# Optimization experiments

Measured on AMD Instinct MI355X. Metric: run time of the kernel, lower is better.

Reference implementation:

```python
import jax, jax.numpy as jnp
import numpy as np

S, E, H, D, F = 2048, 1280, 16, 80, 5120
EPS = 1e-6


def _ln(x, g, b):
    m = x.mean(-1, keepdims=True)
    v = x.var(-1, keepdims=True)
    return (x - m) * jax.lax.rsqrt(v + EPS) * g + b


def _rotate_half(x):
    x1, x2 = jnp.split(x, 2, axis=-1)
    return jnp.concatenate([-x2, x1], axis=-1)


def _quick_gelu(x):
    return x * jax.nn.sigmoid(1.702 * x)


def setup_inputs() -> dict:
    key = jax.random.key(0)
    ks = jax.random.split(key, 12)
    inp = {
        "hidden_states": jax.random.normal(ks[0], (S, E), jnp.float32),
        "attention_mask": jnp.ones((1, 1, S, S), jnp.bool_),
        "cos": jax.random.uniform(ks[1], (S, D), jnp.float32),
        "sin": jax.random.uniform(ks[2], (S, D), jnp.float32),
        "ln1_g": jnp.ones((E,), jnp.float32),
        "ln1_b": jnp.zeros((E,), jnp.float32),
        "ln2_g": jnp.ones((E,), jnp.float32),
        "ln2_b": jnp.zeros((E,), jnp.float32),
        "w_qkv": jax.random.normal(ks[3], (E, 3 * E), jnp.float32) * (E ** -0.5),
        "b_qkv": jax.random.normal(ks[4], (3 * E,), jnp.float32) * 0.02,
        "w_o": jax.random.normal(ks[5], (E, E), jnp.float32) * (E ** -0.5),
        "b_o": jax.random.normal(ks[6], (E,), jnp.float32) * 0.02,
        "w_fc1": jax.random.normal(ks[7], (E, F), jnp.float32) * (E ** -0.5),
        "b_fc1": jax.random.normal(ks[8], (F,), jnp.float32) * 0.02,
        "w_fc2": jax.random.normal(ks[9], (F, E), jnp.float32) * (F ** -0.5),
        "b_fc2": jax.random.normal(ks[10], (E,), jnp.float32) * 0.02,
    }
    return inp


def reference(hidden_states, attention_mask, cos, sin, ln1_g, ln1_b, ln2_g, ln2_b,
              w_qkv, b_qkv, w_o, b_o, w_fc1, b_fc1, w_fc2, b_fc2):
    x = hidden_states  # [S, E]
    h = _ln(x, ln1_g, ln1_b)
    qkv = h @ w_qkv + b_qkv  # [S, 3E]
    q, k, v = jnp.split(qkv, 3, axis=-1)
    q = q.reshape(S, H, D)
    k = k.reshape(S, H, D)
    v = v.reshape(S, H, D)
    # rotary in fp32, cos/sin broadcast over head axis: [S, 1, D]
    c = cos[:, None, :].astype(jnp.float32)
    s = sin[:, None, :].astype(jnp.float32)
    qf, kf = q.astype(jnp.float32), k.astype(jnp.float32)
    q = (qf * c + _rotate_half(qf) * s).astype(q.dtype)
    k = (kf * c + _rotate_half(kf) * s).astype(k.dtype)
    # attention scores [H, S, S]
    scores = jnp.einsum('shd,thd->hst', q, k) / np.float32(np.sqrt(D))
    scores = jnp.where(attention_mask[0], scores, jnp.finfo(scores.dtype).min)
    probs = jax.nn.softmax(scores.astype(jnp.float32), axis=-1).astype(q.dtype)
    attn = jnp.einsum('hst,thd->shd', probs, v).reshape(S, E)
    attn = attn @ w_o + b_o
    x = x + attn
    h2 = _ln(x, ln2_g, ln2_b)
    mlp = _quick_gelu(h2 @ w_fc1 + b_fc1) @ w_fc2 + b_fc2
    return x + mlp
```

## Files before the change

kernel.cpp:

```cpp
#include <hip/hip_runtime.h>
#include <stdint.h>
#include <math.h>

#define S_LEN 2048
#define EMB   1280
#define NHEAD 16
#define HDIM  80
#define FDIM  5120

typedef __bf16 bf16x8 __attribute__((ext_vector_type(8)));
typedef float  f32x4  __attribute__((ext_vector_type(4)));
typedef int    i32x4  __attribute__((ext_vector_type(4)));
typedef unsigned short u16x8 __attribute__((ext_vector_type(8)));
typedef unsigned short u16x4 __attribute__((ext_vector_type(4)));

__device__ __forceinline__ float b2f(unsigned short u) {
    union { float f; unsigned int i; } x; x.i = ((unsigned int)u) << 16; return x.f;
}
__device__ __forceinline__ unsigned short f2b(float f) {
    union { float f; unsigned int i; } x; x.f = f;
    unsigned int r = x.i + 0x7FFFu + ((x.i >> 16) & 1u);
    return (unsigned short)(r >> 16);
}

__device__ __forceinline__ float wave_rsum(float v) {
    #pragma unroll
    for (int o = 32; o; o >>= 1) v += __shfl_down(v, o);
    return v;
}

typedef const __attribute__((address_space(1))) unsigned int* as1_u32p;
typedef __attribute__((address_space(3))) unsigned int* as3_u32p;
__device__ __forceinline__ void gload16(const unsigned short* g, unsigned short* l) {
    __builtin_amdgcn_global_load_lds((as1_u32p)g, (as3_u32p)l, 16, 0, 0);
}

__global__ __launch_bounds__(256) void transpose_conv_kernel(
    const float* __restrict__ in, unsigned short* __restrict__ out,
    int R, int C)
{
    __shared__ unsigned short tile[64][65];
    int c0 = blockIdx.x * 64, r0 = blockIdx.y * 64;
    int tx = threadIdx.x & 63, ty = threadIdx.x >> 6;
    #pragma unroll
    for (int j = 0; j < 16; ++j) {
        int row = ty + j * 4;
        tile[row][tx] = f2b(in[(size_t)(r0 + row) * C + c0 + tx]);
    }
    __syncthreads();
    #pragma unroll
    for (int j = 0; j < 16; ++j) {
        int row = ty + j * 4;
        out[(size_t)(c0 + row) * R + r0 + tx] = tile[tx][row];
    }
}

__global__ __launch_bounds__(256) void ln_kernel(
    const float* __restrict__ x,
    const float* __restrict__ g,
    const float* __restrict__ b,
    unsigned short* __restrict__ out)
{
    int row = blockIdx.x, tid = threadIdx.x;
    int lane = tid & 63, wave = tid >> 6;
    const float* xr = x + (size_t)row * EMB;
    float v[5], s = 0.f, ss = 0.f;
    #pragma unroll
    for (int i = 0; i < 5; ++i) {
        float f = xr[tid + i * 256];
        v[i] = f; s += f; ss += f * f;
    }
    s = wave_rsum(s); ss = wave_rsum(ss);
    __shared__ float rs[4], rss[4];
    if (lane == 0) { rs[wave] = s; rss[wave] = ss; }
    __syncthreads();
    float st  = rs[0] + rs[1] + rs[2] + rs[3];
    float sst = rss[0] + rss[1] + rss[2] + rss[3];
    float mean = st * (1.0f / EMB);
    float var  = sst * (1.0f / EMB) - mean * mean;
    float inv  = rsqrtf(var + 1e-6f);
    unsigned short* orow = out + (size_t)row * EMB;
    #pragma unroll
    for (int i = 0; i < 5; ++i) {
        int c = tid + i * 256;
        orow[c] = f2b((v[i] - mean) * inv * g[c] + b[c]);
    }
}

template<int EPI, int OM, int NT, int SPLIT>
__global__ __launch_bounds__(256) void gemm_kernel(
    const unsigned short* __restrict__ A,
    const unsigned short* __restrict__ Bt,
    const float* __restrict__ bias,
    const float* __restrict__ res,
    void* __restrict__ Cv,
    int M, int N, int K)
{
    __shared__ __align__(16) unsigned short As[2][128 * 32];
    __shared__ __align__(16) unsigned short Bs[2][NT * 32 * 32];

    int tid = threadIdx.x;
    int lane = tid & 63, wave = tid >> 6;
    int m0 = blockIdx.x * 128, n0 = blockIdx.y * (NT * 32);
    int wm = (wave >> 1) * 64, wn = (wave & 1) * (NT * 16);
    int kc = K / SPLIT;
    int kbeg = blockIdx.z * kc;

    f32x4 acc[4][NT];
    #pragma unroll
    for (int i = 0; i < 4; ++i)
        #pragma unroll
        for (int j = 0; j < NT; ++j)
            acc[i][j] = (f32x4){0.f, 0.f, 0.f, 0.f};

    const unsigned short* Ap0 = A  + (size_t)(m0 + (tid >> 2)) * K + (tid & 3) * 8 + kbeg;
    const unsigned short* Ap1 = Ap0 + (size_t)64 * K;
    const unsigned short* Bp0 = Bt + (size_t)(n0 + (tid >> 2)) * K + (tid & 3) * 8 + kbeg;
    const unsigned short* Bp1 = Bp0 + (size_t)64 * K;

    int arow = lane & 15, aq = (lane >> 4) * 8;
    int aoff[4], boff[NT];
    #pragma unroll
    for (int i = 0; i < 4; ++i)
        aoff[i] = (wm + i * 16 + arow) * 32 + aq;
    #pragma unroll
    for (int i = 0; i < NT; ++i)
        boff[i] = (wn + i * 16 + arow) * 32 + aq;

    for (int k0 = 0; k0 < kc; k0 += 64) {
        __syncthreads();
        gload16(Ap0 + k0,      &As[0][tid * 8]);
        gload16(Ap1 + k0,      &As[0][2048 + tid * 8]);
        gload16(Bp0 + k0,      &Bs[0][tid * 8]);
        if (NT == 4) gload16(Bp1 + k0, &Bs[0][2048 + tid * 8]);
        gload16(Ap0 + k0 + 32, &As[1][tid * 8]);
        gload16(Ap1 + k0 + 32, &As[1][2048 + tid * 8]);
        gload16(Bp0 + k0 + 32, &Bs[1][tid * 8]);
        if (NT == 4) gload16(Bp1 + k0 + 32, &Bs[1][2048 + tid * 8]);
        __syncthreads();

        #pragma unroll
        for (int p = 0; p < 2; ++p) {
            bf16x8 af[4], bfm[NT];
            #pragma unroll
            for (int i = 0; i < 4; ++i)
                af[i] = *(const bf16x8*)&As[p][aoff[i]];
            #pragma unroll
            for (int i = 0; i < NT; ++i)
                bfm[i] = *(const bf16x8*)&Bs[p][boff[i]];
            #pragma unroll
            for (int mi = 0; mi < 4; ++mi)
                #pragma unroll
                for (int ni = 0; ni < NT; ++ni)
                    acc[mi][ni] = __builtin_amdgcn_mfma_f32_16x16x32_bf16(
                        af[mi], bfm[ni], acc[mi][ni], 0, 0, 0);
        }
    }

    int col = lane & 15;
    int rbase = (lane >> 4) * 4;
    #pragma unroll
    for (int ni = 0; ni < NT; ++ni) {
        int gn = n0 + wn + ni * 16 + col;
        float bv = (OM == 2) ? 0.f : bias[gn];
        #pragma unroll
        for (int mi = 0; mi < 4; ++mi) {
            int gm = m0 + wm + mi * 16 + rbase;
            #pragma unroll
            for (int r = 0; r < 4; ++r) {
                float v = acc[mi][ni][r] + bv;
                if (OM != 2) {
                    if (EPI == 1) v = v / (1.0f + expf(-1.702f * v));
                    if (EPI == 2) v += res[(size_t)(gm + r) * N + gn];
                }
                if (OM == 2)
                    ((float*)Cv)[((size_t)blockIdx.z * M + gm + r) * N + gn] = v;
                else if (OM == 1)
                    ((float*)Cv)[(size_t)(gm + r) * N + gn] = v;
                else
                    ((unsigned short*)Cv)[(size_t)(gm + r) * N + gn] = f2b(v);
            }
        }
    }
}

__global__ __launch_bounds__(256) void reduce4_kernel(
    const float* __restrict__ part,
    const float* __restrict__ res,
    const float* __restrict__ bias,
    float* __restrict__ out)
{
    size_t i4 = ((size_t)blockIdx.x * 256 + threadIdx.x) * 4;
    int colb = (int)(i4 % EMB);
    f32x4 a = *(const f32x4*)&res[i4];
    f32x4 bv = *(const f32x4*)&bias[colb];
    a += bv;
    const size_t slice = (size_t)S_LEN * EMB;
    #pragma unroll
    for (int z = 0; z < 4; ++z)
        a += *(const f32x4*)&part[z * slice + i4];
    *(f32x4*)&out[i4] = a;
}

__global__ __launch_bounds__(256) void ropev_kernel(
    const unsigned short* __restrict__ qkv,
    const float* __restrict__ cosb,
    const float* __restrict__ sinb,
    unsigned short* __restrict__ q_out,
    unsigned short* __restrict__ k_out,
    unsigned short* __restrict__ vt)
{
    __shared__ unsigned short qT[64 * 84];
    __shared__ unsigned short kT[64 * 84];
    __shared__ unsigned short vT[64 * 84];

    int h = blockIdx.x >> 5, stile = blockIdx.x & 31;
    int s0 = stile * 64;
    int tid = threadIdx.x;

    u16x4 qr[5], kr[5];
    #pragma unroll
    for (int i = 0; i < 5; ++i) {
        int u = tid + i * 256;
        int row = u / 20, col = (u % 20) * 4;
        const unsigned short* base = qkv + (size_t)(s0 + row) * (3 * EMB) + h * HDIM + col;
        qr[i] = *(const u16x4*)base;
        kr[i] = *(const u16x4*)(base + EMB);
        u16x4 v4 = *(const u16x4*)(base + 2 * EMB);
        *(u16x4*)&qT[row * 84 + col] = qr[i];
        *(u16x4*)&kT[row * 84 + col] = kr[i];
        *(u16x4*)&vT[row * 84 + col] = v4;
    }
    __syncthreads();

    #pragma unroll
    for (int i = 0; i < 5; ++i) {
        int u = tid + i * 256;
        int row = u / 20, col = (u % 20) * 4;
        int pcol = (col < 40) ? col + 40 : col - 40;
        float sgn = (col < 40) ? -1.f : 1.f;
        u16x4 qp = *(const u16x4*)&qT[row * 84 + pcol];
        u16x4 kp = *(const u16x4*)&kT[row * 84 + pcol];
        f32x4 c4 = *(const f32x4*)&cosb[(size_t)(s0 + row) * HDIM + col];
        f32x4 s4 = *(const f32x4*)&sinb[(size_t)(s0 + row) * HDIM + col];
        u16x4 qo, ko;
        #pragma unroll
        for (int j = 0; j < 4; ++j) {
            qo[j] = f2b(b2f(qr[i][j]) * c4[j] + sgn * b2f(qp[j]) * s4[j]);
            ko[j] = f2b(b2f(kr[i][j]) * c4[j] + sgn * b2f(kp[j]) * s4[j]);
        }
        size_t o = ((size_t)h * S_LEN + s0 + row) * HDIM + col;
        *(u16x4*)&q_out[o] = qo;
        *(u16x4*)&k_out[o] = ko;
    }
    #pragma unroll
    for (int i = 0; i < 5; ++i) {
        int w = tid + i * 256;
        int d = w >> 4, c4i = (w & 15) * 4;
        u16x4 pk;
        #pragma unroll
        for (int j = 0; j < 4; ++j) pk[j] = vT[(c4i + j) * 84 + d];
        *(u16x4*)(vt + ((size_t)h * HDIM + d) * S_LEN + s0 + c4i) = pk;
    }
}

__global__ __launch_bounds__(256) void fattn_kernel(
    const unsigned short* __restrict__ q,
    const unsigned short* __restrict__ k,
    const unsigned short* __restrict__ vt,
    unsigned short* __restrict__ out)
{
    __shared__ __align__(16) unsigned short Qs[64 * 96];
    __shared__ __align__(16) unsigned short Ks[2][64 * 96];
    __shared__ __align__(16) unsigned short Vs[2][80 * 72];
    __shared__ __align__(16) unsigned short Pt[4 * 16 * 72];

    int tid = threadIdx.x;
    int lane = tid & 63, wave = tid >> 6;
    int arow = lane & 15, quad = lane >> 4;
    int h = blockIdx.x >> 5, qb = blockIdx.x & 31;
    int s0 = qb * 64;
    const float c = 0.16129856f;

    const unsigned short* qbase = q + ((size_t)h * S_LEN + s0) * HDIM;
    const unsigned short* kbase = k + (size_t)h * S_LEN * HDIM;
    const unsigned short* vbase = vt + (size_t)h * HDIM * S_LEN;

    #pragma unroll
    for (int i = 0; i < 5; ++i) {
        int u = tid + i * 256;
        int row = u / 20, col = (u % 20) * 4;
        *(u16x4*)&Qs[row * 96 + col] = *(const u16x4*)(qbase + u * 4);
    }
    {
        int zr = tid >> 2, zc = 80 + (tid & 3) * 4;
        *(u16x4*)&Qs[zr * 96 + zc]    = (u16x4){0, 0, 0, 0};
        *(u16x4*)&Ks[0][zr * 96 + zc] = (u16x4){0, 0, 0, 0};
        *(u16x4*)&Ks[1][zr * 96 + zc] = (u16x4){0, 0, 0, 0};
    }

    u16x4 kreg[5], vreg[5];
    #pragma unroll
    for (int i = 0; i < 5; ++i) {
        int u = tid + i * 256;
        kreg[i] = *(const u16x4*)(kbase + u * 4);
        vreg[i] = *(const u16x4*)(vbase + (size_t)(u >> 4) * S_LEN + (u & 15) * 4);
    }
    #pragma unroll
    for (int i = 0; i < 5; ++i) {
        int u = tid + i * 256;
        *(u16x4*)&Ks[0][(u / 20) * 96 + (u % 20) * 4] = kreg[i];
        *(u16x4*)&Vs[0][(u >> 4) * 72 + (u & 15) * 4] = vreg[i];
    }
    #pragma unroll
    for (int i = 0; i < 5; ++i) {
        int u = tid + i * 256;
        kreg[i] = *(const u16x4*)(kbase + (size_t)64 * HDIM + u * 4);
        vreg[i] = *(const u16x4*)(vbase + (size_t)(u >> 4) * S_LEN + 64 + (u & 15) * 4);
    }
    __syncthreads();

    int pw = wave * 16 * 72;
    float m_run = -3e38f;
    float l_run = 0.f;
    f32x4 o[5];
    #pragma unroll
    for (int di = 0; di < 5; ++di) o[di] = (f32x4){0.f, 0.f, 0.f, 0.f};

    const int NIT = S_LEN / 64;
    for (int it = 0; it < NIT; ++it) {
        int cur = it & 1;
        if (it + 1 < NIT) {
            int nb = (it + 1) & 1;
            #pragma unroll
            for (int i = 0; i < 5; ++i) {
                int u = tid + i * 256;
                *(u16x4*)&Ks[nb][(u / 20) * 96 + (u % 20) * 4] = kreg[i];
                *(u16x4*)&Vs[nb][(u >> 4) * 72 + (u & 15) * 4] = vreg[i];
            }
        }
        if (it + 2 < NIT) {
            int t0 = (it + 2) * 64;
            #pragma unroll
            for (int i = 0; i < 5; ++i) {
                int u = tid + i * 256;
                kreg[i] = *(const u16x4*)(kbase + (size_t)t0 * HDIM + u * 4);
                vreg[i] = *(const u16x4*)(vbase + (size_t)(u >> 4) * S_LEN + t0 + (u & 15) * 4);
            }
        }

        f32x4 sc[4];
        #pragma unroll
        for (int ni = 0; ni < 4; ++ni) sc[ni] = (f32x4){0.f, 0.f, 0.f, 0.f};
        #pragma unroll
        for (int kk = 0; kk < 3; ++kk) {
            bf16x8 bq = *(const bf16x8*)&Qs[(wave * 16 + arow) * 96 + kk * 32 + quad * 8];
            #pragma unroll
            for (int ni = 0; ni < 4; ++ni) {
                bf16x8 ak = *(const bf16x8*)&Ks[cur][(ni * 16 + arow) * 96 + kk * 32 + quad * 8];
                sc[ni] = __builtin_amdgcn_mfma_f32_16x16x32_bf16(ak, bq, sc[ni], 0, 0, 0);
            }
        }

        float tm = -3e38f;
        #pragma unroll
        for (int ni = 0; ni < 4; ++ni)
            #pragma unroll
            for (int r = 0; r < 4; ++r) tm = fmaxf(tm, sc[ni][r]);
        tm = fmaxf(tm, __shfl_xor(tm, 16));
        tm = fmaxf(tm, __shfl_xor(tm, 32));
        float mn = fmaxf(m_run, tm);
        float alpha = exp2f((m_run - mn) * c);
        m_run = mn;
        float mc = mn * c;
        float rs = 0.f;
        #pragma unroll
        for (int ni = 0; ni < 4; ++ni) {
            #pragma unroll
            for (int r = 0; r < 4; ++r) {
                float p = exp2f(sc[ni][r] * c - mc);
                sc[ni][r] = p;
                rs += p;
            }
        }
        rs += __shfl_xor(rs, 16);
        rs += __shfl_xor(rs, 32);
        l_run = l_run * alpha + rs;

        #pragma unroll
        for (int ni = 0; ni < 4; ++ni) {
            u16x4 pk;
            #pragma unroll
            for (int r = 0; r < 4; ++r) {
                __bf16 pb = (__bf16)sc[ni][r];
                pk[r] = *(unsigned short*)&pb;
            }
            *(u16x4*)&Pt[pw + arow * 72 + ni * 16 + quad * 4] = pk;
        }

        float al[4];
        #pragma unroll
        for (int r = 0; r < 4; ++r)
            al[r] = __shfl(alpha, (lane & 48) | (quad * 4 + r));
        #pragma unroll
        for (int di = 0; di < 5; ++di)
            #pragma unroll
            for (int r = 0; r < 4; ++r) o[di][r] *= al[r];

        #pragma unroll
        for (int kk = 0; kk < 2; ++kk) {
            bf16x8 ap = *(const bf16x8*)&Pt[pw + arow * 72 + kk * 32 + quad * 8];
            #pragma unroll
            for (int di = 0; di < 5; ++di) {
                bf16x8 bv = *(const bf16x8*)&Vs[cur][(di * 16 + arow) * 72 + kk * 32 + quad * 8];
                o[di] = __builtin_amdgcn_mfma_f32_16x16x32_bf16(ap, bv, o[di], 0, 0, 0);
            }
        }

        __syncthreads();
    }

    float inv[4];
    #pragma unroll
    for (int r = 0; r < 4; ++r)
        inv[r] = 1.f / __shfl(l_run, (lane & 48) | (quad * 4 + r));
    #pragma unroll
    for (int r = 0; r < 4; ++r) {
        int gq = s0 + wave * 16 + quad * 4 + r;
        unsigned short* op = out + (size_t)gq * EMB + h * HDIM;
        #pragma unroll
        for (int di = 0; di < 5; ++di)
            op[di * 16 + arow] = f2b(o[di][r] * inv[r]);
    }
}

extern "C" void kernel_launch(void* const* d_in, const int* in_sizes, int n_in,
                              void* d_out, int out_size, void* d_ws, size_t ws_size,
                              hipStream_t stream)
{
    const float* hidden = (const float*)d_in[0];
    const float* cosb  = (const float*)d_in[2];
    const float* sinb  = (const float*)d_in[3];
    const float* ln1g  = (const float*)d_in[4];
    const float* ln1b  = (const float*)d_in[5];
    const float* ln2g  = (const float*)d_in[6];
    const float* ln2b  = (const float*)d_in[7];
    const float* w_qkv = (const float*)d_in[8];
    const float* b_qkv = (const float*)d_in[9];
    const float* w_o   = (const float*)d_in[10];
    const float* b_o   = (const float*)d_in[11];
    const float* w_fc1 = (const float*)d_in[12];
    const float* b_fc1 = (const float*)d_in[13];
    const float* w_fc2 = (const float*)d_in[14];
    const float* b_fc2 = (const float*)d_in[15];

    char* ws = (char*)d_ws;
    size_t off = 0;
    auto alloc = [&](size_t bytes) -> void* {
        void* p = (void*)(ws + off);
        off += (bytes + 255) & ~(size_t)255;
        return p;
    };
    unsigned short* wT_qkv = (unsigned short*)alloc((size_t)3840 * 1280 * 2);
    unsigned short* wT_o   = (unsigned short*)alloc((size_t)1280 * 1280 * 2);
    unsigned short* wT_fc1 = (unsigned short*)alloc((size_t)5120 * 1280 * 2);
    unsigned short* wT_fc2 = (unsigned short*)alloc((size_t)1280 * 5120 * 2);
    unsigned short* h1     = (unsigned short*)alloc((size_t)S_LEN * EMB * 2);
    unsigned short* qkv    = (unsigned short*)alloc((size_t)S_LEN * 3 * EMB * 2);
    unsigned short* q_r    = (unsigned short*)alloc((size_t)S_LEN * EMB * 2);
    unsigned short* k_r    = (unsigned short*)alloc((size_t)S_LEN * EMB * 2);
    unsigned short* vt_g   = (unsigned short*)alloc((size_t)S_LEN * EMB * 2);
    unsigned short* attn_o = (unsigned short*)alloc((size_t)S_LEN * EMB * 2);
    float*          x1     = (float*)alloc((size_t)S_LEN * EMB * 4);
    unsigned short* h2     = (unsigned short*)alloc((size_t)S_LEN * EMB * 2);
    unsigned short* mlp1   = (unsigned short*)alloc((size_t)S_LEN * FDIM * 2);
    float* fc2part = (float*)h1;

    transpose_conv_kernel<<<dim3(3840 / 64, 1280 / 64), 256, 0, stream>>>(w_qkv, wT_qkv, 1280, 3840);
    transpose_conv_kernel<<<dim3(1280 / 64, 1280 / 64), 256, 0, stream>>>(w_o,   wT_o,   1280, 1280);
    transpose_conv_kernel<<<dim3(5120 / 64, 1280 / 64), 256, 0, stream>>>(w_fc1, wT_fc1, 1280, 5120);
    transpose_conv_kernel<<<dim3(1280 / 64, 5120 / 64), 256, 0, stream>>>(w_fc2, wT_fc2, 5120, 1280);

    ln_kernel<<<S_LEN, 256, 0, stream>>>(hidden, ln1g, ln1b, h1);

    gemm_kernel<0, 0, 4, 1><<<dim3(S_LEN / 128, 3840 / 128, 1), 256, 0, stream>>>(
        h1, wT_qkv, b_qkv, nullptr, qkv, S_LEN, 3 * EMB, EMB);

    ropev_kernel<<<NHEAD * (S_LEN / 64), 256, 0, stream>>>(qkv, cosb, sinb, q_r, k_r, vt_g);

    fattn_kernel<<<NHEAD * (S_LEN / 64), 256, 0, stream>>>(q_r, k_r, vt_g, attn_o);

    gemm_kernel<2, 1, 2, 1><<<dim3(S_LEN / 128, 1280 / 64, 1), 256, 0, stream>>>(
        attn_o, wT_o, b_o, hidden, x1, S_LEN, EMB, EMB);

    ln_kernel<<<S_LEN, 256, 0, stream>>>(x1, ln2g, ln2b, h2);

    gemm_kernel<1, 0, 4, 1><<<dim3(S_LEN / 128, FDIM / 128, 1), 256, 0, stream>>>(
        h2, wT_fc1, b_fc1, nullptr, mlp1, S_LEN, FDIM, EMB);

    gemm_kernel<0, 2, 4, 4><<<dim3(S_LEN / 128, 1280 / 128, 4), 256, 0, stream>>>(
        mlp1, wT_fc2, b_fc2, nullptr, fc2part, S_LEN, EMB, FDIM);
    reduce4_kernel<<<(S_LEN * EMB / 4) / 256, 256, 0, stream>>>(
        fc2part, x1, b_fc2, (float*)d_out);
}
```

Baseline: 406.3 us.

## Merge weight transposes, shrink GEMM N-tile to 64, split-K the output projection

The four weight-transpose launches become one kernel that dispatches blocks by index range, removing launch overhead. The GEMM template drops the NT parameter and always uses a 128x64 tile, which doubles grid sizes for the QKV, FC1 and FC2 GEMMs to raise occupancy across CUs, at the cost of less A-tile reuse per block. The output projection now uses split-K=2 writing fp32 partials, followed by a reduce kernel that adds bias and the residual. That adds a partial-buffer round trip and one extra launch.

```diff
diff --git a/kernel.cpp b/kernel.cpp
--- a/kernel.cpp
+++ b/kernel.cpp
@@ -35,13 +35,13 @@
     __builtin_amdgcn_global_load_lds((as1_u32p)g, (as3_u32p)l, 16, 0, 0);
 }
 
-__global__ __launch_bounds__(256) void transpose_conv_kernel(
+__device__ __forceinline__ void trans64(
     const float* __restrict__ in, unsigned short* __restrict__ out,
-    int R, int C)
+    int R, int C, int bx, int by, int tid)
 {
     __shared__ unsigned short tile[64][65];
-    int c0 = blockIdx.x * 64, r0 = blockIdx.y * 64;
-    int tx = threadIdx.x & 63, ty = threadIdx.x >> 6;
+    int c0 = bx * 64, r0 = by * 64;
+    int tx = tid & 63, ty = tid >> 6;
     #pragma unroll
     for (int j = 0; j < 16; ++j) {
         int row = ty + j * 4;
@@ -52,6 +52,27 @@
     for (int j = 0; j < 16; ++j) {
         int row = ty + j * 4;
         out[(size_t)(c0 + row) * R + r0 + tx] = tile[tx][row];
+    }
+}
+
+__global__ __launch_bounds__(256) void transpose4_kernel(
+    const float* __restrict__ w_qkv, unsigned short* __restrict__ wT_qkv,
+    const float* __restrict__ w_o,   unsigned short* __restrict__ wT_o,
+    const float* __restrict__ w_fc1, unsigned short* __restrict__ wT_fc1,
+    const float* __restrict__ w_fc2, unsigned short* __restrict__ wT_fc2)
+{
+    int id = blockIdx.x, tid = threadIdx.x;
+    if (id < 1200) {
+        trans64(w_qkv, wT_qkv, 1280, 3840, id % 60, id / 60, tid);
+    } else if (id < 1600) {
+        int t = id - 1200;
+        trans64(w_o, wT_o, 1280, 1280, t % 20, t / 20, tid);
+    } else if (id < 3200) {
+        int t = id - 1600;
+        trans64(w_fc1, wT_fc1, 1280, 5120, t % 80, t / 80, tid);
+    } else {
+        int t = id - 3200;
+        trans64(w_fc2, wT_fc2, 5120, 1280, t % 20, t / 20, tid);
     }
 }
 
@@ -87,7 +108,7 @@
     }
 }
 
-template<int EPI, int OM, int NT, int SPLIT>
+template<int EPI, int OM, int SPLIT>
 __global__ __launch_bounds__(256) void gemm_kernel(
     const unsigned short* __restrict__ A,
     const unsigned short* __restrict__ Bt,
@@ -97,34 +118,33 @@
     int M, int N, int K)
 {
     __shared__ __align__(16) unsigned short As[2][128 * 32];
-    __shared__ __align__(16) unsigned short Bs[2][NT * 32 * 32];
+    __shared__ __align__(16) unsigned short Bs[2][64 * 32];
 
     int tid = threadIdx.x;
     int lane = tid & 63, wave = tid >> 6;
-    int m0 = blockIdx.x * 128, n0 = blockIdx.y * (NT * 32);
-    int wm = (wave >> 1) * 64, wn = (wave & 1) * (NT * 16);
+    int m0 = blockIdx.x * 128, n0 = blockIdx.y * 64;
+    int wm = (wave >> 1) * 64, wn = (wave & 1) * 32;
     int kc = K / SPLIT;
     int kbeg = blockIdx.z * kc;
 
-    f32x4 acc[4][NT];
+    f32x4 acc[4][2];
     #pragma unroll
     for (int i = 0; i < 4; ++i)
         #pragma unroll
-        for (int j = 0; j < NT; ++j)
+        for (int j = 0; j < 2; ++j)
             acc[i][j] = (f32x4){0.f, 0.f, 0.f, 0.f};
 
     const unsigned short* Ap0 = A  + (size_t)(m0 + (tid >> 2)) * K + (tid & 3) * 8 + kbeg;
     const unsigned short* Ap1 = Ap0 + (size_t)64 * K;
     const unsigned short* Bp0 = Bt + (size_t)(n0 + (tid >> 2)) * K + (tid & 3) * 8 + kbeg;
-    const unsigned short* Bp1 = Bp0 + (size_t)64 * K;
 
     int arow = lane & 15, aq = (lane >> 4) * 8;
-    int aoff[4], boff[NT];
+    int aoff[4], boff[2];
     #pragma unroll
     for (int i = 0; i < 4; ++i)
         aoff[i] = (wm + i * 16 + arow) * 32 + aq;
     #pragma unroll
-    for (int i = 0; i < NT; ++i)
+    for (int i = 0; i < 2; ++i)
         boff[i] = (wn + i * 16 + arow) * 32 + aq;
 
     for (int k0 = 0; k0 < kc; k0 += 64) {
@@ -132,26 +152,24 @@
         gload16(Ap0 + k0,      &As[0][tid * 8]);
         gload16(Ap1 + k0,      &As[0][2048 + tid * 8]);
         gload16(Bp0 + k0,      &Bs[0][tid * 8]);
-        if (NT == 4) gload16(Bp1 + k0, &Bs[0][2048 + tid * 8]);
         gload16(Ap0 + k0 + 32, &As[1][tid * 8]);
         gload16(Ap1 + k0 + 32, &As[1][2048 + tid * 8]);
         gload16(Bp0 + k0 + 32, &Bs[1][tid * 8]);
-        if (NT == 4) gload16(Bp1 + k0 + 32, &Bs[1][2048 + tid * 8]);
         __syncthreads();
 
         #pragma unroll
         for (int p = 0; p < 2; ++p) {
-            bf16x8 af[4], bfm[NT];
+            bf16x8 af[4], bfm[2];
             #pragma unroll
             for (int i = 0; i < 4; ++i)
                 af[i] = *(const bf16x8*)&As[p][aoff[i]];
             #pragma unroll
-            for (int i = 0; i < NT; ++i)
+            for (int i = 0; i < 2; ++i)
                 bfm[i] = *(const bf16x8*)&Bs[p][boff[i]];
             #pragma unroll
             for (int mi = 0; mi < 4; ++mi)
                 #pragma unroll
-                for (int ni = 0; ni < NT; ++ni)
+                for (int ni = 0; ni < 2; ++ni)
                     acc[mi][ni] = __builtin_amdgcn_mfma_f32_16x16x32_bf16(
                         af[mi], bfm[ni], acc[mi][ni], 0, 0, 0);
         }
@@ -160,7 +178,7 @@
     int col = lane & 15;
     int rbase = (lane >> 4) * 4;
     #pragma unroll
-    for (int ni = 0; ni < NT; ++ni) {
+    for (int ni = 0; ni < 2; ++ni) {
         int gn = n0 + wn + ni * 16 + col;
         float bv = (OM == 2) ? 0.f : bias[gn];
         #pragma unroll
@@ -184,7 +202,8 @@
     }
 }
 
-__global__ __launch_bounds__(256) void reduce4_kernel(
+template<int Z>
+__global__ __launch_bounds__(256) void reduceZ_kernel(
     const float* __restrict__ part,
     const float* __restrict__ res,
     const float* __restrict__ bias,
@@ -197,7 +216,7 @@
     a += bv;
     const size_t slice = (size_t)S_LEN * EMB;
     #pragma unroll
-    for (int z = 0; z < 4; ++z)
+    for (int z = 0; z < Z; ++z)
         a += *(const f32x4*)&part[z * slice + i4];
     *(f32x4*)&out[i4] = a;
 }
@@ -474,32 +493,32 @@
     float*          x1     = (float*)alloc((size_t)S_LEN * EMB * 4);
     unsigned short* h2     = (unsigned short*)alloc((size_t)S_LEN * EMB * 2);
     unsigned short* mlp1   = (unsigned short*)alloc((size_t)S_LEN * FDIM * 2);
-    float* fc2part = (float*)h1;
-
-    transpose_conv_kernel<<<dim3(3840 / 64, 1280 / 64), 256, 0, stream>>>(w_qkv, wT_qkv, 1280, 3840);
-    transpose_conv_kernel<<<dim3(1280 / 64, 1280 / 64), 256, 0, stream>>>(w_o,   wT_o,   1280, 1280);
-    transpose_conv_kernel<<<dim3(5120 / 64, 1280 / 64), 256, 0, stream>>>(w_fc1, wT_fc1, 1280, 5120);
-    transpose_conv_kernel<<<dim3(1280 / 64, 5120 / 64), 256, 0, stream>>>(w_fc2, wT_fc2, 5120, 1280);
+    float* partials = (float*)h1;
+
+    transpose4_kernel<<<4800, 256, 0, stream>>>(
+        w_qkv, wT_qkv, w_o, wT_o, w_fc1, wT_fc1, w_fc2, wT_fc2);
 
     ln_kernel<<<S_LEN, 256, 0, stream>>>(hidden, ln1g, ln1b, h1);
 
-    gemm_kernel<0, 0, 4, 1><<<dim3(S_LEN / 128, 3840 / 128, 1), 256, 0, stream>>>(
+    gemm_kernel<0, 0, 1><<<dim3(S_LEN / 128, 3840 / 64, 1), 256, 0, stream>>>(
         h1, wT_qkv, b_qkv, nullptr, qkv, S_LEN, 3 * EMB, EMB);
 
     ropev_kernel<<<NHEAD * (S_LEN / 64), 256, 0, stream>>>(qkv, cosb, sinb, q_r, k_r, vt_g);
 
     fattn_kernel<<<NHEAD * (S_LEN / 64), 256, 0, stream>>>(q_r, k_r, vt_g, attn_o);
 
-    gemm_kernel<2, 1, 2, 1><<<dim3(S_LEN / 128, 1280 / 64, 1), 256, 0, stream>>>(
-        attn_o, wT_o, b_o, hidden, x1, S_LEN, EMB, EMB);
+    gemm_kernel<0, 2, 2><<<dim3(S_LEN / 128, 1280 / 64, 2), 256, 0, stream>>>(
+        attn_o, wT_o, b_o, nullptr, partials, S_LEN, EMB, EMB);
+    reduceZ_kernel<2><<<(S_LEN * EMB / 4) / 256, 256, 0, stream>>>(
+        partials, hidden, b_o, x1);
 
     ln_kernel<<<S_LEN, 256, 0, stream>>>(x1, ln2g, ln2b, h2);
 
-    gemm_kernel<1, 0, 4, 1><<<dim3(S_LEN / 128, FDIM / 128, 1), 256, 0, stream>>>(
+    gemm_kernel<1, 0, 1><<<dim3(S_LEN / 128, FDIM / 64, 1), 256, 0, stream>>>(
         h2, wT_fc1, b_fc1, nullptr, mlp1, S_LEN, FDIM, EMB);
 
-    gemm_kernel<0, 2, 4, 4><<<dim3(S_LEN / 128, 1280 / 128, 4), 256, 0, stream>>>(
-        mlp1, wT_fc2, b_fc2, nullptr, fc2part, S_LEN, EMB, FDIM);
-    reduce4_kernel<<<(S_LEN * EMB / 4) / 256, 256, 0, stream>>>(
-        fc2part, x1, b_fc2, (float*)d_out);
-}
+    gemm_kernel<0, 2, 4><<<dim3(S_LEN / 128, 1280 / 64, 4), 256, 0, stream>>>(
+        mlp1, wT_fc2, b_fc2, nullptr, partials, S_LEN, EMB, FDIM);
+    reduceZ_kernel<4><<<(S_LEN * EMB / 4) / 256, 256, 0, stream>>>(
+        partials, x1, b_fc2, (float*)d_out);
+}
```

Result: no change. 401.7 us (-1.1%).
